# Optimization experiments

Hardware: AMD Instinct MI355X
Metric: run time of the kernel (lower is better)

## Reference

```python
import jax, jax.numpy as jnp
import numpy as np

SENSOR_DIM = 256
MODEL_DIM = 512
NUM_DATASETS = 8


def setup_inputs() -> dict:
    key = jax.random.key(0)
    k1, k2, k3 = jax.random.split(key, 3)
    x = jax.random.normal(k1, (32, 200, 1024), dtype=jnp.float32)
    dataset_id = jax.random.randint(k2, (32,), 0, NUM_DATASETS)
    # Conv1d weight [out_ch, in_ch, k] and bias, as in torch.nn.Conv1d
    W = jax.random.normal(k3, (NUM_DATASETS * MODEL_DIM, SENSOR_DIM, 3), dtype=jnp.float32) * 0.02
    b = jnp.zeros((NUM_DATASETS * MODEL_DIM,), dtype=jnp.float32)
    return {"x": x, "dataset_id": dataset_id, "W": W, "b": b}


def reference(x, dataset_id, W, b):
    B, c_in, T = x.shape
    # DatasetPadding: zero-pad channel dim up to sensor_dim
    if c_in < SENSOR_DIM:
        x = jnp.pad(x, ((0, 0), (0, SENSOR_DIM - c_in), (0, 0)))
    # Conv1d(sensor_dim -> num_datasets*model_dim, kernel=3, padding=1)
    y = jax.lax.conv_general_dilated(
        x, W, window_strides=(1,), padding=((1, 1),),
        dimension_numbers=("NCH", "OIH", "NCH"))
    y = y + b[None, :, None]
    y = jax.nn.gelu(y, approximate=False)  # torch GELU default = exact erf
    # unflatten channels to (num_datasets, model_dim) and select per-example dataset slice
    y = y.reshape(B, NUM_DATASETS, MODEL_DIM, T)
    onehot = jax.nn.one_hot(dataset_id, NUM_DATASETS, dtype=y.dtype)  # [B, D]
    out = jnp.einsum("bdmt,bd->bmt", y, onehot)  # [B, model_dim, T]
    return out
```

## Files before the change

### kernel.cpp

```cpp
#include <hip/hip_runtime.h>


typedef unsigned short u16;
typedef __attribute__((ext_vector_type(8))) short bf16x8;
typedef __attribute__((ext_vector_type(4))) float f32x4;

#define CIN 200
#define CINP 224
#define T 1024
#define BATCH 32
#define MD 512
#define XT_ROWS 1026
#define NCHUNK 7
#define XP_PITCH 202
#define TT 256
#define XROWS (TT + 2)
#define XGRAN (XROWS * 4)
#define WGRAN 1536

__device__ __forceinline__ u16 f2bf(float f) {
    unsigned u = __float_as_uint(f);
    u += 0x7FFFu + ((u >> 16) & 1u);
    return (u16)(u >> 16);
}

__device__ __forceinline__ void g2l16(void* lds, const void* g) {
    __builtin_amdgcn_global_load_lds(
        (const __attribute__((address_space(1))) unsigned int*)(uintptr_t)g,
        (__attribute__((address_space(3))) unsigned int*)(unsigned)(uintptr_t)lds,
        16, 0, 0);
}

__global__ __launch_bounds__(256) void prep(const float* __restrict__ x,
                                            const float* __restrict__ W,
                                            u16* __restrict__ xt,
                                            u16* __restrict__ wt) {
    __shared__ u16 tile[64 * XP_PITCH];
    const int tid = threadIdx.x;
    if (blockIdx.x < 512) {
        const int b  = blockIdx.x >> 4;
        const int bx = blockIdx.x & 15;
        const int t0 = bx * 64;
        const int tl = tid & 63;
        const int w  = tid >> 6;
        const float* xb = x + (size_t)b * CIN * T + t0 + tl;
        for (int i = w; i < CIN; i += 4)
            tile[tl * XP_PITCH + i] = f2bf(xb[(size_t)i * T]);
        __syncthreads();
        u16* xrow = xt + ((size_t)b * XT_ROWS + 1 + t0) * CINP;
        for (int it = 0; it < 16; ++it) {
            int r = it * 4 + w;
            if (tl < 56) {
                ushort4 v = {0, 0, 0, 0};
                if (tl < 50) {
                    const u16* p = tile + r * XP_PITCH + tl * 4;
                    v.x = p[0]; v.y = p[1]; v.z = p[2]; v.w = p[3];
                }
                *(ushort4*)(xrow + (size_t)r * CINP + tl * 4) = v;
            }
        }
        if (bx == 0 && tid < 112)
            ((unsigned*)(xt + (size_t)b * XT_ROWS * CINP))[tid] = 0;
        if (bx == 15 && tid < 112)
            ((unsigned*)(xt + ((size_t)b * XT_ROWS + 1025) * CINP))[tid] = 0;
    } else {
        int idx = (blockIdx.x - 512) * 256 + tid;
        int o = idx / CINP;
        int i = idx - o * CINP;
        const float* wp = W + (size_t)o * 768 + i * 3;
        u16* wo = wt + (size_t)o * 3 * CINP + i;
        float w0 = wp[0], w1 = wp[1], w2 = wp[2];
        wo[0]        = f2bf(w0);
        wo[CINP]     = f2bf(w1);
        wo[2 * CINP] = f2bf(w2);
    }
}

__global__ __launch_bounds__(256, 2) void conv_mfma(const u16* __restrict__ xt,
                                                    const u16* __restrict__ wt,
                                                    const int* __restrict__ dsid,
                                                    const float* __restrict__ bias,
                                                    float* __restrict__ out) {
    __shared__ __align__(16) u16 xs[XGRAN * 8];
    __shared__ __align__(16) u16 wsm[WGRAN * 8];

    const int tid = threadIdx.x;
    const int wave = tid >> 6, lane = tid & 63;
    const int l = lane & 15, quad = lane >> 4;
    const int wm  = (wave & 1) * 64;
    const int wti = (wave >> 1) * 128;

    const int id = blockIdx.x;
    const int tb = (id >> 5) * 8 + (id & 7);
    const int m0 = ((id >> 3) & 3) * 128;
    const int t0 = (tb & 3) * TT;
    const int b  = tb >> 2;
    const int d  = dsid[b];
    const int obase = d * MD + m0;

    f32x4 acc[4][8];
#pragma unroll
    for (int mi = 0; mi < 4; ++mi)
#pragma unroll
        for (int ti = 0; ti < 8; ++ti) acc[mi][ti] = (f32x4){0.f, 0.f, 0.f, 0.f};

    const u16* xbase = xt + ((size_t)b * XT_ROWS + t0) * CINP;
    const u16* wbase = wt + (size_t)obase * 3 * CINP;

    const u16* xsrc[5]; u16* xdst[5];
#pragma unroll
    for (int k = 0; k < 5; ++k) {
        int g = tid + k * 256;
        int r = g >> 2, p = g & 3, s = p ^ ((r >> 1) & 3);
        if (g < XGRAN) { xsrc[k] = xbase + (size_t)r * CINP + s * 8; xdst[k] = xs + (size_t)(g & ~63) * 8; }
        else           { xsrc[k] = xbase;                            xdst[k] = xs; }
    }
    const u16* wsrc[6]; u16* wdst[6];
#pragma unroll
    for (int k = 0; k < 6; ++k) {
        int g = tid + k * 256;
        int p = g & 3, m = (g >> 2) & 127, kk = g >> 9;
        int s = p ^ ((m >> 1) & 3);
        wsrc[k] = wbase + ((size_t)m * 3 + kk) * CINP + s * 8;
        wdst[k] = wsm + (size_t)(g & ~63) * 8;
    }

    for (int c = 0; c < NCHUNK; ++c) {
        const int ic = c * 32;
#pragma unroll
        for (int k = 0; k < 5; ++k)
            if (tid + k * 256 < XGRAN) g2l16(xdst[k], xsrc[k] + ic);
#pragma unroll
        for (int k = 0; k < 6; ++k)
            g2l16(wdst[k], wsrc[k] + ic);
        __syncthreads();

#pragma unroll
        for (int tap = 0; tap < 3; ++tap) {
            bf16x8 a[4];
#pragma unroll
            for (int mi = 0; mi < 4; ++mi) {
                int mr = tap * 128 + wm + mi * 16 + l;
                a[mi] = *(const bf16x8*)(wsm + ((size_t)mr * 4 + (quad ^ ((mr >> 1) & 3))) * 8);
            }
#pragma unroll
            for (int ti = 0; ti < 8; ++ti) {
                int row = wti + ti * 16 + l + tap;
                bf16x8 bv = *(const bf16x8*)(xs + ((size_t)row * 4 + (quad ^ ((row >> 1) & 3))) * 8);
#pragma unroll
                for (int mi = 0; mi < 4; ++mi)
                    acc[mi][ti] = __builtin_amdgcn_mfma_f32_16x16x32_bf16(a[mi], bv, acc[mi][ti], 0, 0, 0);
            }
        }
        __syncthreads();
    }

#pragma unroll
    for (int mi = 0; mi < 4; ++mi) {
        float bv[4];
#pragma unroll
        for (int r = 0; r < 4; ++r)
            bv[r] = bias[obase + wm + mi * 16 + quad * 4 + r];
#pragma unroll
        for (int ti = 0; ti < 8; ++ti) {
            int t = t0 + wti + ti * 16 + l;
#pragma unroll
            for (int r = 0; r < 4; ++r) {
                int m = wm + mi * 16 + quad * 4 + r;
                float v = acc[mi][ti][r] + bv[r];
                float p2 = v * v;
                float z2 = v * fmaf(p2, -0.10295089f, -2.30243665f);
                float e = __builtin_amdgcn_exp2f(z2);
                float g = v * __builtin_amdgcn_rcpf(1.0f + e);
                out[((size_t)(b * MD + m0 + m)) * T + t] = g;
            }
        }
    }
}

extern "C" void kernel_launch(void* const* d_in, const int* in_sizes, int n_in,
                              void* d_out, int out_size, void* d_ws, size_t ws_size,
                              hipStream_t stream) {
    const float* x    = (const float*)d_in[0];
    const int*   dsid = (const int*)d_in[1];
    const float* W    = (const float*)d_in[2];
    const float* bias = (const float*)d_in[3];
    float* out = (float*)d_out;

    u16* xt = (u16*)d_ws;
    u16* wt = xt + (size_t)BATCH * XT_ROWS * CINP;

    prep<<<512 + 3584, 256, 0, stream>>>(x, W, xt, wt);
    conv_mfma<<<512, 256, 0, stream>>>(xt, wt, dsid, bias, out);
}
```

Before: 123.4 us.

## Pre-swizzle weights into MFMA fragment order and double-buffer x tiles

The weight prep now writes bf16 weights in the exact per-lane MFMA A-fragment layout, staged through a shared-memory transpose tile. The conv kernel therefore loads weights straight from global memory into registers with one prefetch ahead, instead of staging them through LDS. The x tile is double-buffered in LDS so the next chunk's async loads overlap the current chunk's MFMAs, which removes one barrier per chunk. s_setprio is also raised around each MFMA group. The costs are more register pressure from holding prefetched A fragments and a dependence on global and L2 latency for the weight loads.

```diff
diff --git a/kernel.cpp b/kernel.cpp
--- a/kernel.cpp
+++ b/kernel.cpp
@@ -16,7 +16,8 @@
 #define TT 256
 #define XROWS (TT + 2)
 #define XGRAN (XROWS * 4)
-#define WGRAN 1536
+#define WOB 256
+#define WF_PER_OB (21 * 512)
 
 __device__ __forceinline__ u16 f2bf(float f) {
     unsigned u = __float_as_uint(f);
@@ -34,10 +35,11 @@
 __global__ __launch_bounds__(256) void prep(const float* __restrict__ x,
                                             const float* __restrict__ W,
                                             u16* __restrict__ xt,
-                                            u16* __restrict__ wt) {
-    __shared__ u16 tile[64 * XP_PITCH];
+                                            u16* __restrict__ wf) {
+    __shared__ __align__(16) unsigned char smem[16 * 673 * 4];
     const int tid = threadIdx.x;
     if (blockIdx.x < 512) {
+        u16* tile = (u16*)smem;
         const int b  = blockIdx.x >> 4;
         const int bx = blockIdx.x & 15;
         const int t0 = bx * 64;
@@ -64,25 +66,33 @@
         if (bx == 15 && tid < 112)
             ((unsigned*)(xt + ((size_t)b * XT_ROWS + 1025) * CINP))[tid] = 0;
     } else {
-        int idx = (blockIdx.x - 512) * 256 + tid;
-        int o = idx / CINP;
-        int i = idx - o * CINP;
-        const float* wp = W + (size_t)o * 768 + i * 3;
-        u16* wo = wt + (size_t)o * 3 * CINP + i;
-        float w0 = wp[0], w1 = wp[1], w2 = wp[2];
-        wo[0]        = f2bf(w0);
-        wo[CINP]     = f2bf(w1);
-        wo[2 * CINP] = f2bf(w2);
+        float* wtile = (float*)smem;
+        const int ob = blockIdx.x - 512;
+        const float* wp = W + (size_t)ob * 16 * 768;
+        for (int j = tid; j < 16 * 672; j += 256) {
+            int o = j / 672, r = j - o * 672;
+            wtile[o * 673 + r] = wp[(size_t)o * 768 + r];
+        }
+        __syncthreads();
+        u16* wo = wf + (size_t)ob * WF_PER_OB;
+        for (int j = tid; j < WF_PER_OB; j += 256) {
+            int e    = j & 7;
+            int lane = (j >> 3) & 63;
+            int kc   = j >> 9;
+            int cc   = kc % 7, k = kc / 7;
+            int l = lane & 15, q = lane >> 4;
+            int i = cc * 32 + q * 8 + e;
+            wo[j] = f2bf(wtile[l * 673 + i * 3 + k]);
+        }
     }
 }
 
 __global__ __launch_bounds__(256, 2) void conv_mfma(const u16* __restrict__ xt,
-                                                    const u16* __restrict__ wt,
+                                                    const u16* __restrict__ wf,
                                                     const int* __restrict__ dsid,
                                                     const float* __restrict__ bias,
                                                     float* __restrict__ out) {
-    __shared__ __align__(16) u16 xs[XGRAN * 8];
-    __shared__ __align__(16) u16 wsm[WGRAN * 8];
+    __shared__ __align__(16) u16 xs[2 * XGRAN * 8];
 
     const int tid = threadIdx.x;
     const int wave = tid >> 6, lane = tid & 63;
@@ -105,7 +115,7 @@
         for (int ti = 0; ti < 8; ++ti) acc[mi][ti] = (f32x4){0.f, 0.f, 0.f, 0.f};
 
     const u16* xbase = xt + ((size_t)b * XT_ROWS + t0) * CINP;
-    const u16* wbase = wt + (size_t)obase * 3 * CINP;
+    const u16* wfw = wf + (size_t)((obase + wm) >> 4) * WF_PER_OB + lane * 8;
 
     const u16* xsrc[5]; u16* xdst[5];
 #pragma unroll
@@ -115,59 +125,63 @@
         if (g < XGRAN) { xsrc[k] = xbase + (size_t)r * CINP + s * 8; xdst[k] = xs + (size_t)(g & ~63) * 8; }
         else           { xsrc[k] = xbase;                            xdst[k] = xs; }
     }
-    const u16* wsrc[6]; u16* wdst[6];
-#pragma unroll
-    for (int k = 0; k < 6; ++k) {
-        int g = tid + k * 256;
-        int p = g & 3, m = (g >> 2) & 127, kk = g >> 9;
-        int s = p ^ ((m >> 1) & 3);
-        wsrc[k] = wbase + ((size_t)m * 3 + kk) * CINP + s * 8;
-        wdst[k] = wsm + (size_t)(g & ~63) * 8;
-    }
-
+
+    auto stage = [&](int bsel, int c) {
+        const int ic  = c * 32;
+        const int off = bsel * (XGRAN * 8);
+#pragma unroll
+        for (int k = 0; k < 5; ++k)
+            if (tid + k * 256 < XGRAN) g2l16(xdst[k] + off, xsrc[k] + ic);
+    };
+    auto loadw = [&](bf16x8* dst, int tap, int c) {
+#pragma unroll
+        for (int mi = 0; mi < 4; ++mi)
+            dst[mi] = *(const bf16x8*)(wfw + (size_t)((mi * 21 + tap * 7 + c) << 9));
+    };
+
+    bf16x8 acur[4], anxt[4];
+    stage(0, 0);
+    loadw(acur, 0, 0);
+    __syncthreads();
+
+#pragma unroll
     for (int c = 0; c < NCHUNK; ++c) {
-        const int ic = c * 32;
-#pragma unroll
-        for (int k = 0; k < 5; ++k)
-            if (tid + k * 256 < XGRAN) g2l16(xdst[k], xsrc[k] + ic);
-#pragma unroll
-        for (int k = 0; k < 6; ++k)
-            g2l16(wdst[k], wsrc[k] + ic);
-        __syncthreads();
-
+        const int bsel = c & 1;
+        const u16* xb = xs + bsel * (XGRAN * 8);
 #pragma unroll
         for (int tap = 0; tap < 3; ++tap) {
-            bf16x8 a[4];
-#pragma unroll
-            for (int mi = 0; mi < 4; ++mi) {
-                int mr = tap * 128 + wm + mi * 16 + l;
-                a[mi] = *(const bf16x8*)(wsm + ((size_t)mr * 4 + (quad ^ ((mr >> 1) & 3))) * 8);
+            if (tap == 2 && c + 1 < NCHUNK) stage(bsel ^ 1, c + 1);
+            if (!(tap == 2 && c == NCHUNK - 1))
+                loadw(anxt, (tap == 2 ? 0 : tap + 1), (tap == 2 ? c + 1 : c));
+#pragma unroll
+            for (int ti = 0; ti < 8; ++ti) {
+                int row = wti + tap + ti * 16 + l;
+                bf16x8 bv = *(const bf16x8*)(xb + ((size_t)row * 4 + (quad ^ ((row >> 1) & 3))) * 8);
+                __builtin_amdgcn_s_setprio(1);
+#pragma unroll
+                for (int mi = 0; mi < 4; ++mi)
+                    acc[mi][ti] = __builtin_amdgcn_mfma_f32_16x16x32_bf16(acur[mi], bv, acc[mi][ti], 0, 0, 0);
+                __builtin_amdgcn_s_setprio(0);
             }
 #pragma unroll
-            for (int ti = 0; ti < 8; ++ti) {
-                int row = wti + ti * 16 + l + tap;
-                bf16x8 bv = *(const bf16x8*)(xs + ((size_t)row * 4 + (quad ^ ((row >> 1) & 3))) * 8);
-#pragma unroll
-                for (int mi = 0; mi < 4; ++mi)
-                    acc[mi][ti] = __builtin_amdgcn_mfma_f32_16x16x32_bf16(a[mi], bv, acc[mi][ti], 0, 0, 0);
-            }
-        }
-        __syncthreads();
+            for (int mi = 0; mi < 4; ++mi) acur[mi] = anxt[mi];
+        }
+        if (c + 1 < NCHUNK) __syncthreads();
     }
 
 #pragma unroll
     for (int mi = 0; mi < 4; ++mi) {
-        float bv[4];
+        float bvv[4];
 #pragma unroll
         for (int r = 0; r < 4; ++r)
-            bv[r] = bias[obase + wm + mi * 16 + quad * 4 + r];
+            bvv[r] = bias[obase + wm + mi * 16 + quad * 4 + r];
 #pragma unroll
         for (int ti = 0; ti < 8; ++ti) {
             int t = t0 + wti + ti * 16 + l;
 #pragma unroll
             for (int r = 0; r < 4; ++r) {
                 int m = wm + mi * 16 + quad * 4 + r;
-                float v = acc[mi][ti][r] + bv[r];
+                float v = acc[mi][ti][r] + bvv[r];
                 float p2 = v * v;
                 float z2 = v * fmaf(p2, -0.10295089f, -2.30243665f);
                 float e = __builtin_amdgcn_exp2f(z2);
@@ -188,8 +202,8 @@
     float* out = (float*)d_out;
 
     u16* xt = (u16*)d_ws;
-    u16* wt = xt + (size_t)BATCH * XT_ROWS * CINP;
-
-    prep<<<512 + 3584, 256, 0, stream>>>(x, W, xt, wt);
-    conv_mfma<<<512, 256, 0, stream>>>(xt, wt, dsid, bias, out);
-}
+    u16* wf = xt + (size_t)BATCH * XT_ROWS * CINP;
+
+    prep<<<512 + WOB, 256, 0, stream>>>(x, W, xt, wf);
+    conv_mfma<<<512, 256, 0, stream>>>(xt, wf, dsid, bias, out);
+}
```

After: 124.0 us, median of 2. About the same (+0.4%).
